# Optimization experiments

Measured on AMD Instinct MI355X. Metric: run time of the kernel, lower is better.

The kernel has to match this reference:

```python
import jax, jax.numpy as jnp
import numpy as np

V = 100000   # nodes
E = 3200000  # edges (avg degree 32)
K = 16       # radial filters
T = 4        # atom types


def setup_inputs() -> dict:
    key = jax.random.key(0)
    k1, k2, k3, k4 = jax.random.split(key, 4)
    feat = jax.random.randint(k1, (V, 1), 0, T).astype(jnp.float32)  # atomic-type ids as floats
    distances = jax.random.uniform(k2, (E, 1), jnp.float32) * 12.0   # pairwise distances in [0, 12)
    src = jax.random.randint(k3, (E,), 0, V, dtype=jnp.int32)
    dst = jax.random.randint(k4, (E,), 0, V, dtype=jnp.int32)
    interaction_cutoffs = jnp.full((K,), 12.0, dtype=jnp.float32)
    rbf_kernel_means = jnp.linspace(0.0, 12.0, K).astype(jnp.float32)
    rbf_kernel_scaling = jnp.ones((K,), dtype=jnp.float32)
    features_to_use = jnp.arange(T, dtype=jnp.float32)
    return {
        'feat': feat, 'distances': distances, 'src': src, 'dst': dst,
        'interaction_cutoffs': interaction_cutoffs,
        'rbf_kernel_means': rbf_kernel_means,
        'rbf_kernel_scaling': rbf_kernel_scaling,
        'features_to_use': features_to_use,
    }


def reference(feat, distances, src, dst, interaction_cutoffs,
              rbf_kernel_means, rbf_kernel_scaling, features_to_use):
    d = distances                                    # (E, 1)
    # RadialPooling: rbf * cosine cutoff, broadcast (E,1) vs (K,) -> (E,K)
    rbf = jnp.exp(-rbf_kernel_scaling * (d - rbf_kernel_means) ** 2)
    cos_v = 0.5 * (jnp.cos(jnp.pi * d / interaction_cutoffs) + 1.0)
    he = rbf * jnp.where(d <= interaction_cutoffs, cos_v, jnp.zeros_like(cos_v))  # (E, K)
    # one-hot atom-type features (V, T)
    hv = (feat == features_to_use[None, :]).astype(distances.dtype)
    # gather src features, outer product with radial features -> (E, T, K)
    msg = hv[src][:, :, None] * he[:, None, :]
    # scatter-sum to destination nodes -> (V, T*K)
    out = jax.ops.segment_sum(msg.reshape(msg.shape[0], -1), dst, num_segments=V)
    return out
```

## Files before the change

### kernel.cpp

```cpp
#include <hip/hip_runtime.h>
#include <math.h>

#define NV 100000
#define NE 3200000
#define NK 16
#define NT 4
#define NB 782
#define NG 8
#define NBG (NB * NG)
#define BCAP 6016
#define SCH 8192
#define NCHUNK ((NE + SCH - 1) / SCH)
#define PI_F 3.14159265358979323846f
#define LOG2E_F 1.4426950408889634f


__global__ __launch_bounds__(256) void zero_out_kernel(float4* __restrict__ out, int n4) {
    int i = blockIdx.x * blockDim.x + threadIdx.x;
    if (i < n4) out[i] = make_float4(0.f, 0.f, 0.f, 0.f);
}

__global__ __launch_bounds__(256) void atomic_conv_edge_kernel(
    const float* __restrict__ feat, const float* __restrict__ dist,
    const int* __restrict__ src, const int* __restrict__ dst,
    const float* __restrict__ cutoffs, const float* __restrict__ means,
    const float* __restrict__ scaling, const float* __restrict__ feats_use,
    float* __restrict__ out)
{
    int e = blockIdx.x * blockDim.x + threadIdx.x;
    if (e >= NE) return;
    float d = dist[e];
    int s = src[e];
    int v = dst[e];
    float fv = feat[s];
    int ty = 0;
#pragma unroll
    for (int t = 1; t < NT; ++t) if (fv == feats_use[t]) ty = t;
    float* o = out + (size_t)v * (NT * NK) + (size_t)ty * NK;
#pragma unroll
    for (int k = 0; k < NK; ++k) {
        float c = cutoffs[k], m = means[k], sc = scaling[k];
        float dm = d - m;
        float rbf = __expf(-sc * dm * dm);
        float cosv = 0.5f * (__cosf(PI_F * d / c) + 1.0f);
        float he = (d <= c) ? rbf * cosv : 0.0f;
        __hip_atomic_fetch_add(o + k, he, __ATOMIC_RELAXED, __HIP_MEMORY_SCOPE_AGENT);
    }
}


__global__ __launch_bounds__(256) void zero_counts_kernel(int* __restrict__ p, int n) {
    int i = blockIdx.x * blockDim.x + threadIdx.x;
    if (i < n) p[i] = 0;
}

__global__ __launch_bounds__(256) void hist_kernel(const int4* __restrict__ dst4,
                                                   int* __restrict__ counts) {
    __shared__ int h[NB];
    for (int i = threadIdx.x; i < NB; i += 256) h[i] = 0;
    __syncthreads();
    const int nqTot = NE / 4;
    int q0 = blockIdx.x * (SCH / 4);
    int nq = nqTot - q0;
    if (nq > SCH / 4) nq = SCH / 4;
    for (int i = threadIdx.x; i < nq; i += 256) {
        int4 v = dst4[q0 + i];
        atomicAdd(&h[v.x >> 7], 1);
        atomicAdd(&h[v.y >> 7], 1);
        atomicAdd(&h[v.z >> 7], 1);
        atomicAdd(&h[v.w >> 7], 1);
    }
    __syncthreads();
    int g = blockIdx.x & (NG - 1);
    for (int i = threadIdx.x; i < NB; i += 256) {
        int c = h[i];
        if (c) atomicAdd(&counts[i * NG + g], c);
    }
}

__global__ __launch_bounds__(1024) void scan_kernel(const int* __restrict__ counts,
                                                    int* __restrict__ offsets,
                                                    int* __restrict__ cursors) {
    __shared__ int s[1024];
    const int CH = (NBG + 1023) / 1024;
    int t = threadIdx.x;
    int base = t * CH;
    int loc[CH];
    int sum = 0;
#pragma unroll
    for (int i = 0; i < CH; ++i) {
        int idx = base + i;
        int v = (idx < NBG) ? counts[idx] : 0;
        loc[i] = sum;
        sum += v;
    }
    s[t] = sum;
    __syncthreads();
#pragma unroll
    for (int off = 1; off < 1024; off <<= 1) {
        int v = (t >= off) ? s[t - off] : 0;
        __syncthreads();
        s[t] += v;
        __syncthreads();
    }
    int excl = (t > 0) ? s[t - 1] : 0;
#pragma unroll
    for (int i = 0; i < CH; ++i) {
        int idx = base + i;
        if (idx < NBG) {
            int o = excl + loc[i];
            offsets[idx] = o;
            cursors[idx] = o;
        }
    }
    if (t == 1023) offsets[NBG] = NE;
}

__global__ __launch_bounds__(256) void scatter_kernel(
    const float* __restrict__ feat, const float* __restrict__ dist,
    const int* __restrict__ src, const int* __restrict__ dst,
    const float* __restrict__ feats_use,
    int* __restrict__ cursors, unsigned* __restrict__ payload)
{
    __shared__ unsigned pld[SCH];
    __shared__ unsigned short bkt[SCH];
    __shared__ int hist[NB];
    __shared__ int base[NB];

    int t = threadIdx.x;
    int g = blockIdx.x & (NG - 1);
    int chunkBase = blockIdx.x * SCH;
    int n = NE - chunkBase;
    if (n > SCH) n = SCH;

    float f1 = feats_use[1], f2 = feats_use[2], f3 = feats_use[3];

    for (int i = t; i < NB; i += 256) hist[i] = 0;
    __syncthreads();

    for (int i = t; i < n; i += 256) {
        int e = chunkBase + i;
        float d = dist[e];
        int s = src[e];
        int v = dst[e];
        float fv = feat[s];
        int ty = (fv == f1) ? 1 : (fv == f2) ? 2 : (fv == f3) ? 3 : 0;
        int b = v >> 7;
        unsigned packed = (__float_as_uint(d) & 0xFFFFFE00u) |
                          ((unsigned)ty << 7) | (unsigned)(v & 127);
        pld[i] = packed;
        bkt[i] = (unsigned short)b;
        atomicAdd(&hist[b], 1);
    }
    __syncthreads();

    for (int i = t; i < NB; i += 256) {
        int c = hist[i];
        base[i] = c ? __hip_atomic_fetch_add(&cursors[i * NG + g], c,
                                             __ATOMIC_RELAXED, __HIP_MEMORY_SCOPE_AGENT)
                    : 0;
        hist[i] = 0;
    }
    __syncthreads();

    for (int i = t; i < n; i += 256) {
        int b = bkt[i];
        int lp = atomicAdd(&hist[b], 1);
        payload[base[b] + lp] = pld[i];
    }
}

__global__ __launch_bounds__(256, 3) void reduce_kernel(
    const unsigned* __restrict__ payload, const int* __restrict__ offsets,
    const float* __restrict__ cutoffs, const float* __restrict__ means,
    const float* __restrict__ scaling, float* __restrict__ out)
{
    __shared__ unsigned raw[BCAP];
    __shared__ unsigned srt[BCAP];
    __shared__ int scn[256];
    __shared__ int cur[256];
    __shared__ int coff[257];

    int b = blockIdx.x;
    int t = threadIdx.x;
    int s0 = offsets[b * NG];
    int s1 = offsets[(b + 1) * NG];

    float m_[NK], nsc_[NK], c_[NK], w_[NK], c1_[NK];
    bool uniformC = true;
#pragma unroll
    for (int k = 0; k < NK; ++k) {
        m_[k] = means[k];
        nsc_[k] = -scaling[k];
        c_[k] = cutoffs[k];
        w_[k] = PI_F / cutoffs[k];
        c1_[k] = -scaling[k] * LOG2E_F;
        uniformC = uniformC && (cutoffs[k] == cutoffs[0]);
    }
    float c0 = c_[0];
    float w0 = w_[0];

    float accA[NK], accB[NK];
#pragma unroll
    for (int k = 0; k < NK; ++k) { accA[k] = 0.f; accB[k] = 0.f; }

    for (int base = s0; base < s1; base += BCAP) {
        int n = s1 - base;
        if (n > BCAP) n = BCAP;

        for (int i = t; i < n; i += 256) raw[i] = payload[base + i];
        scn[t] = 0;
        __syncthreads();

        for (int i = t; i < n; i += 256) {
            unsigned p = raw[i];
            int key = ((p & 127) << 1) | ((p >> 8) & 1);
            atomicAdd(&scn[key], 1);
        }
        __syncthreads();

        int x = scn[t];
#pragma unroll
        for (int off2 = 1; off2 < 256; off2 <<= 1) {
            int v = (t >= off2) ? scn[t - off2] : 0;
            __syncthreads();
            scn[t] += v;
            __syncthreads();
        }
        int excl = scn[t] - x;
        coff[t] = excl;
        cur[t] = excl;
        if (t == 0) coff[256] = n;
        __syncthreads();

        for (int i = t; i < n; i += 256) {
            unsigned p = raw[i];
            int key = ((p & 127) << 1) | ((p >> 8) & 1);
            int pos = atomicAdd(&cur[key], 1);
            srt[pos] = p;
        }
        __syncthreads();

        int e0 = coff[t];
        int e1 = coff[t + 1];
        if (uniformC) {
#pragma unroll 2
            for (int i = e0; i < e1; ++i) {
                unsigned p = srt[i];
                float d = __uint_as_float(p & 0xFFFFFE00u);
                int typar = (p >> 7) & 1;
                float cv = 0.5f * (__cosf(w0 * d) + 1.0f);
                cv = (d <= c0) ? cv : 0.0f;
                float mA = typar ? 0.0f : cv;
                float mB = typar ? cv : 0.0f;
#pragma unroll
                for (int k = 0; k < NK; ++k) {
                    float dm = d - m_[k];
                    float e = exp2f(c1_[k] * (dm * dm));
                    accA[k] = fmaf(e, mA, accA[k]);
                    accB[k] = fmaf(e, mB, accB[k]);
                }
            }
        } else {
            for (int i = e0; i < e1; ++i) {
                unsigned p = srt[i];
                float d = __uint_as_float(p & 0xFFFFFE00u);
                int typar = (p >> 7) & 1;
                float he[NK];
#pragma unroll
                for (int k = 0; k < NK; ++k) {
                    float dm = d - m_[k];
                    float rbf = __expf(nsc_[k] * dm * dm);
                    float cosv = 0.5f * (__cosf(w_[k] * d) + 1.0f);
                    he[k] = (d <= c_[k]) ? rbf * cosv : 0.0f;
                }
                if (typar == 0) {
#pragma unroll
                    for (int k = 0; k < NK; ++k) accA[k] += he[k];
                } else {
#pragma unroll
                    for (int k = 0; k < NK; ++k) accB[k] += he[k];
                }
            }
        }
        __syncthreads();
    }

    int node = b * 128 + (t >> 1);
    if (node < NV) {
        int h = t & 1;
        float4* o = (float4*)(out + (size_t)node * 64 + h * 32);
#pragma unroll
        for (int k = 0; k < 4; ++k)
            o[k] = make_float4(accA[4 * k], accA[4 * k + 1], accA[4 * k + 2], accA[4 * k + 3]);
#pragma unroll
        for (int k = 0; k < 4; ++k)
            o[4 + k] = make_float4(accB[4 * k], accB[4 * k + 1], accB[4 * k + 2], accB[4 * k + 3]);
    }
}

extern "C" void kernel_launch(void* const* d_in, const int* in_sizes, int n_in,
                              void* d_out, int out_size, void* d_ws, size_t ws_size,
                              hipStream_t stream) {
    const float* feat      = (const float*)d_in[0];
    const float* dist      = (const float*)d_in[1];
    const int*   src       = (const int*)d_in[2];
    const int*   dst       = (const int*)d_in[3];
    const float* cutoffs   = (const float*)d_in[4];
    const float* means     = (const float*)d_in[5];
    const float* scaling   = (const float*)d_in[6];
    const float* feats_use = (const float*)d_in[7];
    float* out = (float*)d_out;

    size_t off = 0;
    auto alloc = [&](size_t bytes) {
        size_t cur = off;
        off = (off + bytes + 255) & ~(size_t)255;
        return cur;
    };
    size_t o_counts  = alloc((size_t)NBG * 4);
    size_t o_offsets = alloc((size_t)(NBG + 1) * 4);
    size_t o_cursors = alloc((size_t)NBG * 4);
    size_t o_payload = alloc((size_t)NE * 4);
    size_t needed = off;

    if (ws_size < needed) {
        int n4 = out_size / 4;
        zero_out_kernel<<<(n4 + 255) / 256, 256, 0, stream>>>((float4*)out, n4);
        atomic_conv_edge_kernel<<<(NE + 255) / 256, 256, 0, stream>>>(
            feat, dist, src, dst, cutoffs, means, scaling, feats_use, out);
        return;
    }

    char* ws = (char*)d_ws;
    int* counts  = (int*)(ws + o_counts);
    int* offsets = (int*)(ws + o_offsets);
    int* cursors = (int*)(ws + o_cursors);
    unsigned* payload = (unsigned*)(ws + o_payload);

    zero_counts_kernel<<<(NBG + 255) / 256, 256, 0, stream>>>(counts, NBG);

    hist_kernel<<<NCHUNK, 256, 0, stream>>>((const int4*)dst, counts);

    scan_kernel<<<1, 1024, 0, stream>>>(counts, offsets, cursors);

    scatter_kernel<<<NCHUNK, 256, 0, stream>>>(
        feat, dist, src, dst, feats_use, cursors, payload);

    reduce_kernel<<<NB, 256, 0, stream>>>(
        payload, offsets, cutoffs, means, scaling, out);
}
```

Baseline: 213.3 us.

## Shrink reduce buckets to 64 nodes, one thread per node-type pair

Dst-node buckets shrink from 128 to 64 nodes, which doubles the bucket count. The payload key now packs the node and the full atom type into 8 bits, so each reduce thread owns a single (node, type) pair with one 16-wide accumulator instead of two. This drops the FMAs that were multiplied by zero and halves the accumulator registers, which allows higher occupancy; the launch-bounds occupancy hint is removed. It doubles the number of reduce blocks and the histogram/scan sizes, and each thread now does the exp work for only its own type's edges, so per-edge cost stays the same while wasted work is removed.

```diff
diff --git a/kernel.cpp b/kernel.cpp
--- a/kernel.cpp
+++ b/kernel.cpp
@@ -5,10 +5,11 @@
 #define NE 3200000
 #define NK 16
 #define NT 4
-#define NB 782
+#define NBK 64
+#define NB 1563
 #define NG 8
 #define NBG (NB * NG)
-#define BCAP 6016
+#define BCAP 3072
 #define SCH 8192
 #define NCHUNK ((NE + SCH - 1) / SCH)
 #define PI_F 3.14159265358979323846f
@@ -65,10 +66,10 @@
     if (nq > SCH / 4) nq = SCH / 4;
     for (int i = threadIdx.x; i < nq; i += 256) {
         int4 v = dst4[q0 + i];
-        atomicAdd(&h[v.x >> 7], 1);
-        atomicAdd(&h[v.y >> 7], 1);
-        atomicAdd(&h[v.z >> 7], 1);
-        atomicAdd(&h[v.w >> 7], 1);
+        atomicAdd(&h[v.x >> 6], 1);
+        atomicAdd(&h[v.y >> 6], 1);
+        atomicAdd(&h[v.z >> 6], 1);
+        atomicAdd(&h[v.w >> 6], 1);
     }
     __syncthreads();
     int g = blockIdx.x & (NG - 1);
@@ -145,9 +146,9 @@
         int v = dst[e];
         float fv = feat[s];
         int ty = (fv == f1) ? 1 : (fv == f2) ? 2 : (fv == f3) ? 3 : 0;
-        int b = v >> 7;
+        int b = v >> 6;
         unsigned packed = (__float_as_uint(d) & 0xFFFFFE00u) |
-                          ((unsigned)ty << 7) | (unsigned)(v & 127);
+                          ((unsigned)(v & 63) << 2) | (unsigned)ty;
         pld[i] = packed;
         bkt[i] = (unsigned short)b;
         atomicAdd(&hist[b], 1);
@@ -170,7 +171,7 @@
     }
 }
 
-__global__ __launch_bounds__(256, 3) void reduce_kernel(
+__global__ __launch_bounds__(256) void reduce_kernel(
     const unsigned* __restrict__ payload, const int* __restrict__ offsets,
     const float* __restrict__ cutoffs, const float* __restrict__ means,
     const float* __restrict__ scaling, float* __restrict__ out)
@@ -186,23 +187,20 @@
     int s0 = offsets[b * NG];
     int s1 = offsets[(b + 1) * NG];
 
-    float m_[NK], nsc_[NK], c_[NK], w_[NK], c1_[NK];
+    float m_[NK], c1_[NK];
     bool uniformC = true;
 #pragma unroll
     for (int k = 0; k < NK; ++k) {
         m_[k] = means[k];
-        nsc_[k] = -scaling[k];
-        c_[k] = cutoffs[k];
-        w_[k] = PI_F / cutoffs[k];
         c1_[k] = -scaling[k] * LOG2E_F;
         uniformC = uniformC && (cutoffs[k] == cutoffs[0]);
     }
-    float c0 = c_[0];
-    float w0 = w_[0];
-
-    float accA[NK], accB[NK];
-#pragma unroll
-    for (int k = 0; k < NK; ++k) { accA[k] = 0.f; accB[k] = 0.f; }
+    float c0 = cutoffs[0];
+    float w0 = PI_F / c0;
+
+    float acc[NK];
+#pragma unroll
+    for (int k = 0; k < NK; ++k) acc[k] = 0.f;
 
     for (int base = s0; base < s1; base += BCAP) {
         int n = s1 - base;
@@ -213,8 +211,7 @@
         __syncthreads();
 
         for (int i = t; i < n; i += 256) {
-            unsigned p = raw[i];
-            int key = ((p & 127) << 1) | ((p >> 8) & 1);
+            int key = raw[i] & 255;
             atomicAdd(&scn[key], 1);
         }
         __syncthreads();
@@ -235,7 +232,7 @@
 
         for (int i = t; i < n; i += 256) {
             unsigned p = raw[i];
-            int key = ((p & 127) << 1) | ((p >> 8) & 1);
+            int key = p & 255;
             int pos = atomicAdd(&cur[key], 1);
             srt[pos] = p;
         }
@@ -248,54 +245,39 @@
             for (int i = e0; i < e1; ++i) {
                 unsigned p = srt[i];
                 float d = __uint_as_float(p & 0xFFFFFE00u);
-                int typar = (p >> 7) & 1;
                 float cv = 0.5f * (__cosf(w0 * d) + 1.0f);
                 cv = (d <= c0) ? cv : 0.0f;
-                float mA = typar ? 0.0f : cv;
-                float mB = typar ? cv : 0.0f;
 #pragma unroll
                 for (int k = 0; k < NK; ++k) {
                     float dm = d - m_[k];
                     float e = exp2f(c1_[k] * (dm * dm));
-                    accA[k] = fmaf(e, mA, accA[k]);
-                    accB[k] = fmaf(e, mB, accB[k]);
+                    acc[k] = fmaf(e, cv, acc[k]);
                 }
             }
         } else {
             for (int i = e0; i < e1; ++i) {
                 unsigned p = srt[i];
                 float d = __uint_as_float(p & 0xFFFFFE00u);
-                int typar = (p >> 7) & 1;
-                float he[NK];
 #pragma unroll
                 for (int k = 0; k < NK; ++k) {
                     float dm = d - m_[k];
-                    float rbf = __expf(nsc_[k] * dm * dm);
-                    float cosv = 0.5f * (__cosf(w_[k] * d) + 1.0f);
-                    he[k] = (d <= c_[k]) ? rbf * cosv : 0.0f;
-                }
-                if (typar == 0) {
-#pragma unroll
-                    for (int k = 0; k < NK; ++k) accA[k] += he[k];
-                } else {
-#pragma unroll
-                    for (int k = 0; k < NK; ++k) accB[k] += he[k];
+                    float rbf = __expf(-scaling[k] * dm * dm);
+                    float cosv = 0.5f * (__cosf(PI_F * d / cutoffs[k]) + 1.0f);
+                    float he = (d <= cutoffs[k]) ? rbf * cosv : 0.0f;
+                    acc[k] += he;
                 }
             }
         }
         __syncthreads();
     }
 
-    int node = b * 128 + (t >> 1);
+    int node = b * NBK + (t >> 2);
     if (node < NV) {
-        int h = t & 1;
-        float4* o = (float4*)(out + (size_t)node * 64 + h * 32);
+        int ty = t & 3;
+        float4* o = (float4*)(out + (size_t)node * 64 + ty * 16);
 #pragma unroll
         for (int k = 0; k < 4; ++k)
-            o[k] = make_float4(accA[4 * k], accA[4 * k + 1], accA[4 * k + 2], accA[4 * k + 3]);
-#pragma unroll
-        for (int k = 0; k < 4; ++k)
-            o[4 + k] = make_float4(accB[4 * k], accB[4 * k + 1], accB[4 * k + 2], accB[4 * k + 3]);
+            o[k] = make_float4(acc[4 * k], acc[4 * k + 1], acc[4 * k + 2], acc[4 * k + 3]);
     }
 }
 
```

Result: slower. 228.1 us (+6.9%).
